# Kernel optimization log

Hardware: AMD Instinct MI355X
Metric: run time of the kernel (lower is better)

The kernel has to match this reference:

```python
import jax, jax.numpy as jnp
import numpy as np

EPS = 1e-12  # torch F.normalize eps

def setup_inputs() -> dict:
    key = jax.random.key(0)
    k1, k2, k3 = jax.random.split(key, 3)
    b, c, h, w = 4, 192, 128, 128
    x = jax.random.normal(k1, (b, c, h, w), dtype=jnp.float32)
    # torch Linear weight transposed: x @ W_qkv, columns ordered [q | k | v]
    W_qkv = jax.random.normal(k2, (c, 3 * c), dtype=jnp.float32) * (1.0 / np.sqrt(c))
    W_lin = jax.random.normal(k3, (c, c), dtype=jnp.float32) * (1.0 / np.sqrt(c))
    sigma = jnp.ones((1, 1), dtype=jnp.float32)
    return {"x": x, "W_qkv": W_qkv, "W_lin": W_lin, "sigma": sigma}

def _l2norm_tokens(t):
    # normalize along token axis (dim=1 of [b, hw, c]), torch-style eps clamp
    n = jnp.sqrt(jnp.sum(t * t, axis=1, keepdims=True))
    return t / jnp.maximum(n, EPS)

def reference(x, W_qkv, W_lin, sigma):
    b, c, h, w = x.shape
    xt = jnp.transpose(x.reshape(b, c, h * w), (0, 2, 1))  # [b, hw, c]
    qkv = xt @ W_qkv                                        # [b, hw, 3c]
    q, k, v = jnp.split(qkv, 3, axis=-1)
    q = _l2norm_tokens(q)
    k = _l2norm_tokens(k)
    attn = jnp.einsum('bnc,bnd->bcd', k, q) * sigma[0, 0]   # [b, c, c]
    attn = jax.nn.softmax(attn, axis=-1)
    out = jnp.einsum('bnc,bcd->bnd', v, attn) @ W_lin       # [b, hw, c]
    return jnp.transpose(out, (0, 2, 1)).reshape(b, c, h, w)
```

## Files before the change

### kernel.cpp

```cpp
#include <hip/hip_runtime.h>

#define CCH 192
#define HWN 16384
#define NB  4
#define SPLIT 16

typedef __attribute__((ext_vector_type(8))) short bf16x8;
typedef __attribute__((ext_vector_type(4))) float f32x4;


__device__ __forceinline__ ushort f2bf(float f) {
  union { float f; unsigned u; } v; v.f = f;
  return (ushort)((v.u + 0x7fffu + ((v.u >> 16) & 1u)) >> 16);
}

__device__ __forceinline__ float wsum(float v) {
#pragma unroll
  for (int off = 32; off > 0; off >>= 1) v += __shfl_xor(v, off, 64);
  return v;
}
__device__ __forceinline__ float wmax(float v) {
#pragma unroll
  for (int off = 32; off > 0; off >>= 1) v = fmaxf(v, __shfl_xor(v, off, 64));
  return v;
}

__global__ __launch_bounds__(256) void k0_wconv(const float* __restrict__ Wqkv, ushort* __restrict__ Wb) {
  int j0 = blockIdx.x * 64, c0 = blockIdx.y * 64;
  __shared__ float L[64][65];
  int t = threadIdx.x;
#pragma unroll
  for (int p = 0; p < 4; ++p) {
    int idx = t + 256 * p;
    int row = idx >> 4, col = (idx & 15) << 2;
    float4 v = *reinterpret_cast<const float4*>(&Wqkv[(size_t)(c0 + row) * 576 + j0 + col]);
    L[row][col] = v.x; L[row][col + 1] = v.y; L[row][col + 2] = v.z; L[row][col + 3] = v.w;
  }
  __syncthreads();
#pragma unroll
  for (int p = 0; p < 4; ++p) {
    int idx = t + 256 * p;
    int jrow = idx >> 4, c4 = (idx & 15) << 2;
    ushort4 o;
    o.x = f2bf(L[c4 + 0][jrow]);
    o.y = f2bf(L[c4 + 1][jrow]);
    o.z = f2bf(L[c4 + 2][jrow]);
    o.w = f2bf(L[c4 + 3][jrow]);
    *reinterpret_cast<ushort4*>(&Wb[(size_t)(j0 + jrow) * CCH + c0 + c4]) = o;
  }
}

__global__ __launch_bounds__(256, 2) void k12_qkv(
    const float* __restrict__ x, const ushort* __restrict__ Wb,
    ushort* __restrict__ Tqk2, ushort* __restrict__ Vt2, float* __restrict__ norm2p)
{
  int z = blockIdx.y;
  const float* xb = x + (size_t)z * CCH * HWN;
  ushort* Tb2 = Tqk2 + (size_t)z * 384 * HWN;
  ushort* Vb2 = Vt2 + (size_t)z * HWN * CCH;
  float* npb = norm2p + (size_t)z * 256 * 384;
  int nt = blockIdx.x;
  int n0 = nt * 64;
  __shared__ __align__(16) ushort SM[13056];
  ushort* FR = SM;
  int t = threadIdx.x, l = t & 63, w = t >> 6;
  int lg = l >> 4, lr = l & 15;

  {
    int nl = l;
    const float* xrow = xb + n0 + nl;
    int frbase = (nl >> 4) * 3072 + (nl & 15) * 8;
#pragma unroll
    for (int tile = 0; tile < 6; ++tile) {
      int chunk = tile * 4 + w;
      int c0 = chunk * 8;
      float v[8];
#pragma unroll
      for (int j = 0; j < 8; ++j)
        v[j] = xrow[(size_t)(c0 + j) * HWN];
      unsigned q0 = (unsigned)f2bf(v[0]) | ((unsigned)f2bf(v[1]) << 16);
      unsigned q1 = (unsigned)f2bf(v[2]) | ((unsigned)f2bf(v[3]) << 16);
      unsigned q2 = (unsigned)f2bf(v[4]) | ((unsigned)f2bf(v[5]) << 16);
      unsigned q3 = (unsigned)f2bf(v[6]) | ((unsigned)f2bf(v[7]) << 16);
      *reinterpret_cast<int4*>(&FR[frbase + chunk * 128]) = make_int4(q0, q1, q2, q3);
    }
  }
  __syncthreads();

  bf16x8 a[6][4];
#pragma unroll
  for (int k = 0; k < 6; ++k)
#pragma unroll
    for (int m = 0; m < 4; ++m)
      a[k][m] = *reinterpret_cast<const bf16x8*>(&FR[m * 3072 + (4 * k + lg) * 128 + lr * 8]);

#pragma unroll
  for (int jt = 0; jt < 3; ++jt) {
    f32x4 acc[4][3] = {};
#pragma unroll
    for (int k = 0; k < 6; ++k) {
      bf16x8 b[3];
#pragma unroll
      for (int f = 0; f < 3; ++f)
        b[f] = *reinterpret_cast<const bf16x8*>(
            &Wb[(size_t)(jt * 192 + w * 48 + 16 * f + lr) * CCH + 32 * k + 8 * lg]);
#pragma unroll
      for (int m = 0; m < 4; ++m)
#pragma unroll
        for (int f = 0; f < 3; ++f)
          acc[m][f] = __builtin_amdgcn_mfma_f32_16x16x32_bf16(a[k][m], b[f], acc[m][f], 0, 0, 0);
    }

    if (jt == 2) {
      __syncthreads();
      ushort* Ep = SM;
#pragma unroll
      for (int m = 0; m < 4; ++m)
#pragma unroll
        for (int f = 0; f < 3; ++f) {
          int cl = w * 48 + 16 * f + lr;
          int nb = 16 * m + 4 * lg;
#pragma unroll
          for (int r = 0; r < 4; ++r)
            Ep[(nb + r) * 200 + cl] = f2bf(acc[m][f][r]);
        }
      __syncthreads();
      int nblk = n0 >> 4;
#pragma unroll
      for (int p = 0; p < 6; ++p) {
        int ii = t + 256 * p;
        int nq = ii & 15, n16 = ii / 384, cg = (ii - n16 * 384) >> 4;
        int4 v = *reinterpret_cast<const int4*>(&Ep[(n16 * 16 + nq) * 200 + cg * 8]);
        size_t off = (size_t)(nblk + n16) * (16 * CCH) + cg * 128 + nq * 8;
        *reinterpret_cast<int4*>(&Vb2[off]) = v;
      }
    } else {
      int jb16 = jt * 12 + 3 * w;
#pragma unroll
      for (int f = 0; f < 3; ++f) {
        float sq = 0.f;
#pragma unroll
        for (int m = 0; m < 4; ++m)
#pragma unroll
          for (int r = 0; r < 4; ++r) sq += acc[m][f][r] * acc[m][f][r];
        sq += __shfl_xor(sq, 16, 64);
        sq += __shfl_xor(sq, 32, 64);
        if (lg == 0) {
          int j = jt * 192 + w * 48 + 16 * f + lr;
          npb[(size_t)nt * 384 + j] = sq;
        }
#pragma unroll
        for (int m = 0; m < 4; ++m) {
          uint2 pk;
          pk.x = (unsigned)f2bf(acc[m][f][0]) | ((unsigned)f2bf(acc[m][f][1]) << 16);
          pk.y = (unsigned)f2bf(acc[m][f][2]) | ((unsigned)f2bf(acc[m][f][3]) << 16);
          size_t off = (size_t)(jb16 + f) * (16 * HWN) +
                       (size_t)(nt * 8 + 2 * m + (lg >> 1)) * 128 + lr * 8 + 4 * (lg & 1);
          *reinterpret_cast<uint2*>(&Tb2[off]) = pk;
        }
      }
    }
  }
}

__global__ __launch_bounds__(256) void k3_invn(const float* __restrict__ norm2p, float* __restrict__ invn) {
  int z = blockIdx.y, j = blockIdx.x;
  const float* npb = norm2p + (size_t)z * 256 * 384;
  int t = threadIdx.x;
  float s = npb[(size_t)t * 384 + j];
  s = wsum(s);
  __shared__ float red[4];
  if ((t & 63) == 0) red[t >> 6] = s;
  __syncthreads();
  if (t == 0) {
    float tot = red[0] + red[1] + red[2] + red[3];
    invn[(size_t)z * 384 + j] = 1.f / fmaxf(sqrtf(tot), 1e-12f);
  }
}

__global__ __launch_bounds__(256) void k4_gram(const ushort* __restrict__ Tqk2, float* __restrict__ Gpart) {
  int z = blockIdx.z;
  const ushort* Tb2 = Tqk2 + (size_t)z * 384 * HWN;
  float* Gb = Gpart + (size_t)z * SPLIT * CCH * CCH;
  int tile = blockIdx.x, chunk = blockIdx.y;
  int ct = tile / 3, dt = tile % 3;
  int t = threadIdx.x, l = t & 63, w = t >> 6;
  int wc = w >> 1, wd = w & 1, lg = l >> 4, lr = l & 15;
  f32x4 acc[2][2] = {};
  for (int s = 0; s < 16; ++s) {
    int nco = chunk * 128 + s * 8;
#pragma unroll
    for (int hh = 0; hh < 2; ++hh) {
      int ko = nco + 4 * hh + lg;
      bf16x8 a[2], bb[2];
#pragma unroll
      for (int m = 0; m < 2; ++m)
        a[m] = *reinterpret_cast<const bf16x8*>(
            &Tb2[(size_t)(12 + 4 * ct + 2 * wc + m) * (16 * HWN) + (size_t)ko * 128 + lr * 8]);
#pragma unroll
      for (int f = 0; f < 2; ++f)
        bb[f] = *reinterpret_cast<const bf16x8*>(
            &Tb2[(size_t)(4 * dt + 2 * wd + f) * (16 * HWN) + (size_t)ko * 128 + lr * 8]);
#pragma unroll
      for (int m = 0; m < 2; ++m)
#pragma unroll
        for (int f = 0; f < 2; ++f)
          acc[m][f] = __builtin_amdgcn_mfma_f32_16x16x32_bf16(a[m], bb[f], acc[m][f], 0, 0, 0);
    }
  }
#pragma unroll
  for (int m = 0; m < 2; ++m)
#pragma unroll
    for (int f = 0; f < 2; ++f)
#pragma unroll
      for (int r = 0; r < 4; ++r)
        Gb[(size_t)(chunk * CCH + ct * 64 + 32 * wc + 16 * m + 4 * lg + r) * CCH +
           dt * 64 + 32 * wd + 16 * f + lr] = acc[m][f][r];
}

__global__ __launch_bounds__(64) void k5_softmax(
    const float* __restrict__ Gpart, const float* __restrict__ invn,
    const float* __restrict__ sigma, float* __restrict__ S)
{
  int c = blockIdx.x, z = blockIdx.y;
  const float* Gb = Gpart + (size_t)z * SPLIT * CCH * CCH;
  const float* inb = invn + (size_t)z * 384;
  float sig = sigma[0];
  float ink = inb[192 + c];
  float lv[3];
#pragma unroll
  for (int r = 0; r < 3; ++r) {
    int d = threadIdx.x + 64 * r;
    float s = 0.f;
    for (int ch = 0; ch < SPLIT; ++ch)
      s += Gb[(size_t)(ch * CCH + c) * CCH + d];
    lv[r] = s * ink * inb[d] * sig;
  }
  float m = fmaxf(lv[0], fmaxf(lv[1], lv[2]));
  m = wmax(m);
  float e[3], tot = 0.f;
#pragma unroll
  for (int r = 0; r < 3; ++r) { e[r] = __expf(lv[r] - m); tot += e[r]; }
  tot = wsum(tot);
  float inv = 1.f / tot;
  float* Sb = S + (size_t)z * CCH * CCH;
#pragma unroll
  for (int r = 0; r < 3; ++r) Sb[(size_t)c * CCH + threadIdx.x + 64 * r] = e[r] * inv;
}

__global__ __launch_bounds__(192) void k6_mlin(
    const float* __restrict__ S, const float* __restrict__ Wlin, ushort* __restrict__ Mt)
{
  int z = blockIdx.y, c = blockIdx.x, e = threadIdx.x;
  const float* Sb = S + (size_t)z * CCH * CCH;
  float s = 0.f;
  for (int d = 0; d < CCH; ++d) s += Sb[(size_t)c * CCH + d] * Wlin[(size_t)d * CCH + e];
  Mt[(size_t)z * CCH * CCH + (size_t)e * CCH + c] = f2bf(s);
}

__global__ __launch_bounds__(256, 2) void k7_out(
    const ushort* __restrict__ Mt, const ushort* __restrict__ Vt2, float* __restrict__ out)
{
  int z = blockIdx.y;
  const ushort* Mb = Mt + (size_t)z * CCH * CCH;
  const ushort* Vb2 = Vt2 + (size_t)z * HWN * CCH;
  float* ob = out + (size_t)z * CCH * HWN;
  int nt = blockIdx.x;
  int n0 = nt * 128;
  int t = threadIdx.x, l = t & 63, w = t >> 6;
  int wn = w >> 1, we = w & 1, lg = l >> 4, lr = l & 15;
  int nblk = n0 >> 4;
  f32x4 acc[3][4][2] = {};
#pragma unroll
  for (int h = 0; h < 2; ++h)
#pragma unroll
    for (int k3 = 0; k3 < 3; ++k3) {
      bf16x8 an[4];
#pragma unroll
      for (int ng = 0; ng < 4; ++ng)
        an[ng] = *reinterpret_cast<const bf16x8*>(
            &Vb2[(size_t)(nblk + 4 * wn + ng) * (16 * CCH) + (12 * h + 4 * k3 + lg) * 128 + lr * 8]);
#pragma unroll
      for (int et = 0; et < 3; ++et) {
        bf16x8 mf[2];
#pragma unroll
        for (int mg = 0; mg < 2; ++mg)
          mf[mg] = *reinterpret_cast<const bf16x8*>(
              &Mb[(size_t)(et * 64 + 32 * we + 16 * mg + lr) * CCH + 96 * h + 32 * k3 + 8 * lg]);
#pragma unroll
        for (int ng = 0; ng < 4; ++ng)
#pragma unroll
          for (int mg = 0; mg < 2; ++mg)
            acc[et][ng][mg] = __builtin_amdgcn_mfma_f32_16x16x32_bf16(an[ng], mf[mg], acc[et][ng][mg], 0, 0, 0);
      }
    }
#pragma unroll
  for (int et = 0; et < 3; ++et)
#pragma unroll
    for (int ng = 0; ng < 4; ++ng)
#pragma unroll
      for (int mg = 0; mg < 2; ++mg)
        *reinterpret_cast<f32x4*>(
            &ob[(size_t)(et * 64 + 32 * we + 16 * mg + lr) * HWN + n0 + 64 * wn + 16 * ng + 4 * lg]) = acc[et][ng][mg];
}

extern "C" void kernel_launch(void* const* d_in, const int* in_sizes, int n_in,
                              void* d_out, int out_size, void* d_ws, size_t ws_size,
                              hipStream_t stream) {
  const float* x     = (const float*)d_in[0];
  const float* Wqkv  = (const float*)d_in[1];
  const float* Wlin  = (const float*)d_in[2];
  const float* sigma = (const float*)d_in[3];
  float* out = (float*)d_out;

  const size_t wbElems = (size_t)576 * CCH;
  const size_t perB =
      (size_t)384 * HWN * 2 +
      (size_t)HWN * CCH * 2 +
      (size_t)256 * 384 * 4 +
      (size_t)384 * 4 +
      (size_t)SPLIT * CCH * CCH * 4 +
      (size_t)CCH * CCH * 4 +
      (size_t)CCH * CCH * 2;
  int per = (ws_size >= wbElems * 2 + (size_t)NB * perB) ? NB : 1;

  ushort* Wb = (ushort*)d_ws;
  k0_wconv<<<dim3(9, 3), 256, 0, stream>>>(Wqkv, Wb);

  for (int b0 = 0; b0 < NB; b0 += per) {
    char* base = (char*)d_ws + wbElems * 2;
    ushort* Tqk2 = (ushort*)base;
    ushort* Vt2  = Tqk2 + (size_t)per * 384 * HWN;
    float* norm2p = (float*)(Vt2 + (size_t)per * HWN * CCH);
    float* invn  = norm2p + (size_t)per * 256 * 384;
    float* Gpart = invn + (size_t)per * 384;
    float* S     = Gpart + (size_t)per * SPLIT * CCH * CCH;
    ushort* Mt   = (ushort*)(S + (size_t)per * CCH * CCH);
    const float* xb = x + (size_t)b0 * CCH * HWN;
    float* ob = out + (size_t)b0 * CCH * HWN;

    k12_qkv   <<<dim3(256, per), 256, 0, stream>>>(xb, Wb, Tqk2, Vt2, norm2p);
    k3_invn   <<<dim3(384, per), 256, 0, stream>>>(norm2p, invn);
    k4_gram   <<<dim3(9, SPLIT, per), 256, 0, stream>>>(Tqk2, Gpart);
    k5_softmax<<<dim3(192, per), 64, 0, stream>>>(Gpart, invn, sigma, S);
    k6_mlin   <<<dim3(192, per), 192, 0, stream>>>(S, Wlin, Mt);
    k7_out    <<<dim3(128, per), 256, 0, stream>>>(Mt, Vt2, ob);
  }
}
```

Baseline: 112.2 us.

## Shrink token tiles to raise grid size across QKV, Gram and output kernels

The QKV projection kernel now processes 32 tokens per block instead of 64, which doubles the grid and the number of partial norm rows. The Gram kernel split goes from 16 to 32 chunks, and the output kernel is retiled to 32 tokens per block with four waves each owning 48 output channels, plus a higher occupancy hint. The workspace batching logic also falls back more gracefully. The aim is to fill the GPU's compute units better and raise occupancy. The cost is less reuse of loaded weights per block and more partial sums to reduce.

```diff
diff --git a/kernel.cpp b/kernel.cpp
--- a/kernel.cpp
+++ b/kernel.cpp
@@ -3,7 +3,7 @@
 #define CCH 192
 #define HWN 16384
 #define NB  4
-#define SPLIT 16
+#define SPLIT 32
 
 typedef __attribute__((ext_vector_type(8))) short bf16x8;
 typedef __attribute__((ext_vector_type(4))) float f32x4;
@@ -58,21 +58,21 @@
   const float* xb = x + (size_t)z * CCH * HWN;
   ushort* Tb2 = Tqk2 + (size_t)z * 384 * HWN;
   ushort* Vb2 = Vt2 + (size_t)z * HWN * CCH;
-  float* npb = norm2p + (size_t)z * 256 * 384;
+  float* npb = norm2p + (size_t)z * 512 * 384;
   int nt = blockIdx.x;
-  int n0 = nt * 64;
-  __shared__ __align__(16) ushort SM[13056];
+  int n0 = nt * 32;
+  __shared__ __align__(16) ushort SM[6400];
   ushort* FR = SM;
   int t = threadIdx.x, l = t & 63, w = t >> 6;
   int lg = l >> 4, lr = l & 15;
 
   {
-    int nl = l;
+    int nl = t & 31, cg = t >> 5;
     const float* xrow = xb + n0 + nl;
     int frbase = (nl >> 4) * 3072 + (nl & 15) * 8;
 #pragma unroll
-    for (int tile = 0; tile < 6; ++tile) {
-      int chunk = tile * 4 + w;
+    for (int tile = 0; tile < 3; ++tile) {
+      int chunk = tile * 8 + cg;
       int c0 = chunk * 8;
       float v[8];
 #pragma unroll
@@ -87,16 +87,16 @@
   }
   __syncthreads();
 
-  bf16x8 a[6][4];
+  bf16x8 a[6][2];
 #pragma unroll
   for (int k = 0; k < 6; ++k)
 #pragma unroll
-    for (int m = 0; m < 4; ++m)
+    for (int m = 0; m < 2; ++m)
       a[k][m] = *reinterpret_cast<const bf16x8*>(&FR[m * 3072 + (4 * k + lg) * 128 + lr * 8]);
 
 #pragma unroll
   for (int jt = 0; jt < 3; ++jt) {
-    f32x4 acc[4][3] = {};
+    f32x4 acc[2][3] = {};
 #pragma unroll
     for (int k = 0; k < 6; ++k) {
       bf16x8 b[3];
@@ -105,7 +105,7 @@
         b[f] = *reinterpret_cast<const bf16x8*>(
             &Wb[(size_t)(jt * 192 + w * 48 + 16 * f + lr) * CCH + 32 * k + 8 * lg]);
 #pragma unroll
-      for (int m = 0; m < 4; ++m)
+      for (int m = 0; m < 2; ++m)
 #pragma unroll
         for (int f = 0; f < 3; ++f)
           acc[m][f] = __builtin_amdgcn_mfma_f32_16x16x32_bf16(a[k][m], b[f], acc[m][f], 0, 0, 0);
@@ -115,7 +115,7 @@
       __syncthreads();
       ushort* Ep = SM;
 #pragma unroll
-      for (int m = 0; m < 4; ++m)
+      for (int m = 0; m < 2; ++m)
 #pragma unroll
         for (int f = 0; f < 3; ++f) {
           int cl = w * 48 + 16 * f + lr;
@@ -125,9 +125,9 @@
             Ep[(nb + r) * 200 + cl] = f2bf(acc[m][f][r]);
         }
       __syncthreads();
-      int nblk = n0 >> 4;
-#pragma unroll
-      for (int p = 0; p < 6; ++p) {
+      int nblk = nt * 2;
+#pragma unroll
+      for (int p = 0; p < 3; ++p) {
         int ii = t + 256 * p;
         int nq = ii & 15, n16 = ii / 384, cg = (ii - n16 * 384) >> 4;
         int4 v = *reinterpret_cast<const int4*>(&Ep[(n16 * 16 + nq) * 200 + cg * 8]);
@@ -140,7 +140,7 @@
       for (int f = 0; f < 3; ++f) {
         float sq = 0.f;
 #pragma unroll
-        for (int m = 0; m < 4; ++m)
+        for (int m = 0; m < 2; ++m)
 #pragma unroll
           for (int r = 0; r < 4; ++r) sq += acc[m][f][r] * acc[m][f][r];
         sq += __shfl_xor(sq, 16, 64);
@@ -150,12 +150,12 @@
           npb[(size_t)nt * 384 + j] = sq;
         }
 #pragma unroll
-        for (int m = 0; m < 4; ++m) {
+        for (int m = 0; m < 2; ++m) {
           uint2 pk;
           pk.x = (unsigned)f2bf(acc[m][f][0]) | ((unsigned)f2bf(acc[m][f][1]) << 16);
           pk.y = (unsigned)f2bf(acc[m][f][2]) | ((unsigned)f2bf(acc[m][f][3]) << 16);
           size_t off = (size_t)(jb16 + f) * (16 * HWN) +
-                       (size_t)(nt * 8 + 2 * m + (lg >> 1)) * 128 + lr * 8 + 4 * (lg & 1);
+                       (size_t)(nt * 4 + 2 * m + (lg >> 1)) * 128 + lr * 8 + 4 * (lg & 1);
           *reinterpret_cast<uint2*>(&Tb2[off]) = pk;
         }
       }
@@ -165,9 +165,9 @@
 
 __global__ __launch_bounds__(256) void k3_invn(const float* __restrict__ norm2p, float* __restrict__ invn) {
   int z = blockIdx.y, j = blockIdx.x;
-  const float* npb = norm2p + (size_t)z * 256 * 384;
+  const float* npb = norm2p + (size_t)z * 512 * 384;
   int t = threadIdx.x;
-  float s = npb[(size_t)t * 384 + j];
+  float s = npb[(size_t)t * 384 + j] + npb[(size_t)(t + 256) * 384 + j];
   s = wsum(s);
   __shared__ float red[4];
   if ((t & 63) == 0) red[t >> 6] = s;
@@ -187,8 +187,8 @@
   int t = threadIdx.x, l = t & 63, w = t >> 6;
   int wc = w >> 1, wd = w & 1, lg = l >> 4, lr = l & 15;
   f32x4 acc[2][2] = {};
-  for (int s = 0; s < 16; ++s) {
-    int nco = chunk * 128 + s * 8;
+  for (int s = 0; s < 8; ++s) {
+    int nco = chunk * 64 + s * 8;
 #pragma unroll
     for (int hh = 0; hh < 2; ++hh) {
       int ko = nco + 4 * hh + lg;
@@ -258,7 +258,7 @@
   Mt[(size_t)z * CCH * CCH + (size_t)e * CCH + c] = f2bf(s);
 }
 
-__global__ __launch_bounds__(256, 2) void k7_out(
+__global__ __launch_bounds__(256, 4) void k7_out(
     const ushort* __restrict__ Mt, const ushort* __restrict__ Vt2, float* __restrict__ out)
 {
   int z = blockIdx.y;
@@ -266,42 +266,35 @@
   const ushort* Vb2 = Vt2 + (size_t)z * HWN * CCH;
   float* ob = out + (size_t)z * CCH * HWN;
   int nt = blockIdx.x;
-  int n0 = nt * 128;
+  int n0 = nt * 32, nblk = nt * 2;
   int t = threadIdx.x, l = t & 63, w = t >> 6;
-  int wn = w >> 1, we = w & 1, lg = l >> 4, lr = l & 15;
-  int nblk = n0 >> 4;
-  f32x4 acc[3][4][2] = {};
+  int lg = l >> 4, lr = l & 15;
+  f32x4 acc[2][3] = {};
 #pragma unroll
   for (int h = 0; h < 2; ++h)
 #pragma unroll
     for (int k3 = 0; k3 < 3; ++k3) {
-      bf16x8 an[4];
-#pragma unroll
-      for (int ng = 0; ng < 4; ++ng)
+      bf16x8 an[2], mf[3];
+#pragma unroll
+      for (int ng = 0; ng < 2; ++ng)
         an[ng] = *reinterpret_cast<const bf16x8*>(
-            &Vb2[(size_t)(nblk + 4 * wn + ng) * (16 * CCH) + (12 * h + 4 * k3 + lg) * 128 + lr * 8]);
-#pragma unroll
-      for (int et = 0; et < 3; ++et) {
-        bf16x8 mf[2];
-#pragma unroll
-        for (int mg = 0; mg < 2; ++mg)
-          mf[mg] = *reinterpret_cast<const bf16x8*>(
-              &Mb[(size_t)(et * 64 + 32 * we + 16 * mg + lr) * CCH + 96 * h + 32 * k3 + 8 * lg]);
-#pragma unroll
-        for (int ng = 0; ng < 4; ++ng)
-#pragma unroll
-          for (int mg = 0; mg < 2; ++mg)
-            acc[et][ng][mg] = __builtin_amdgcn_mfma_f32_16x16x32_bf16(an[ng], mf[mg], acc[et][ng][mg], 0, 0, 0);
-      }
-    }
-#pragma unroll
-  for (int et = 0; et < 3; ++et)
-#pragma unroll
-    for (int ng = 0; ng < 4; ++ng)
-#pragma unroll
-      for (int mg = 0; mg < 2; ++mg)
-        *reinterpret_cast<f32x4*>(
-            &ob[(size_t)(et * 64 + 32 * we + 16 * mg + lr) * HWN + n0 + 64 * wn + 16 * ng + 4 * lg]) = acc[et][ng][mg];
+            &Vb2[(size_t)(nblk + ng) * (16 * CCH) + (12 * h + 4 * k3 + lg) * 128 + lr * 8]);
+#pragma unroll
+      for (int f = 0; f < 3; ++f)
+        mf[f] = *reinterpret_cast<const bf16x8*>(
+            &Mb[(size_t)(w * 48 + 16 * f + lr) * CCH + 96 * h + 32 * k3 + 8 * lg]);
+#pragma unroll
+      for (int ng = 0; ng < 2; ++ng)
+#pragma unroll
+        for (int f = 0; f < 3; ++f)
+          acc[ng][f] = __builtin_amdgcn_mfma_f32_16x16x32_bf16(an[ng], mf[f], acc[ng][f], 0, 0, 0);
+    }
+#pragma unroll
+  for (int ng = 0; ng < 2; ++ng)
+#pragma unroll
+    for (int f = 0; f < 3; ++f)
+      *reinterpret_cast<f32x4*>(
+          &ob[(size_t)(w * 48 + 16 * f + lr) * HWN + n0 + 16 * ng + 4 * lg]) = acc[ng][f];
 }
 
 extern "C" void kernel_launch(void* const* d_in, const int* in_sizes, int n_in,
@@ -317,12 +310,13 @@
   const size_t perB =
       (size_t)384 * HWN * 2 +
       (size_t)HWN * CCH * 2 +
-      (size_t)256 * 384 * 4 +
+      (size_t)512 * 384 * 4 +
       (size_t)384 * 4 +
       (size_t)SPLIT * CCH * CCH * 4 +
       (size_t)CCH * CCH * 4 +
       (size_t)CCH * CCH * 2;
-  int per = (ws_size >= wbElems * 2 + (size_t)NB * perB) ? NB : 1;
+  int per = 4;
+  while (per > 1 && ws_size < wbElems * 2 + (size_t)per * perB) per >>= 1;
 
   ushort* Wb = (ushort*)d_ws;
   k0_wconv<<<dim3(9, 3), 256, 0, stream>>>(Wqkv, Wb);
@@ -332,18 +326,18 @@
     ushort* Tqk2 = (ushort*)base;
     ushort* Vt2  = Tqk2 + (size_t)per * 384 * HWN;
     float* norm2p = (float*)(Vt2 + (size_t)per * HWN * CCH);
-    float* invn  = norm2p + (size_t)per * 256 * 384;
+    float* invn  = norm2p + (size_t)per * 512 * 384;
     float* Gpart = invn + (size_t)per * 384;
     float* S     = Gpart + (size_t)per * SPLIT * CCH * CCH;
     ushort* Mt   = (ushort*)(S + (size_t)per * CCH * CCH);
     const float* xb = x + (size_t)b0 * CCH * HWN;
     float* ob = out + (size_t)b0 * CCH * HWN;
 
-    k12_qkv   <<<dim3(256, per), 256, 0, stream>>>(xb, Wb, Tqk2, Vt2, norm2p);
+    k12_qkv   <<<dim3(512, per), 256, 0, stream>>>(xb, Wb, Tqk2, Vt2, norm2p);
     k3_invn   <<<dim3(384, per), 256, 0, stream>>>(norm2p, invn);
     k4_gram   <<<dim3(9, SPLIT, per), 256, 0, stream>>>(Tqk2, Gpart);
     k5_softmax<<<dim3(192, per), 64, 0, stream>>>(Gpart, invn, sigma, S);
     k6_mlin   <<<dim3(192, per), 192, 0, stream>>>(S, Wlin, Mt);
-    k7_out    <<<dim3(128, per), 256, 0, stream>>>(Mt, Vt2, ob);
-  }
-}
+    k7_out    <<<dim3(512, per), 256, 0, stream>>>(Mt, Vt2, ob);
+  }
+}
```

After: 148.0 us. 1.32x slower.
